# Performance work log

Hardware: AMD Instinct MI355X
Metric: run time of the kernel (lower is better)

Reference implementation:

```python
import jax, jax.numpy as jnp
import numpy as np

# Fixed topology: layer sizes input I, hidden H, output O; memory size M.
B, T, I, H, O, M = 64, 512, 256, 512, 256, 256
HALF = H // 2  # units 0..HALF-1 -> relu, HALF..H-1 -> tanh (activation ids 1 and 3)


def setup_inputs() -> dict:
    key = jax.random.key(0)
    ks = jax.random.split(key, 17)
    w = lambda k, shape: jax.random.normal(k, shape, dtype=jnp.float32) * 0.05
    return {
        "inputs": jax.random.normal(ks[0], (B, T, I), dtype=jnp.float32),
        # computation-graph edge weights (torch Linear: W @ x + b, W is (out,in))
        "W01": w(ks[1], (H, I)), "b01": w(ks[2], (H,)),
        "W12": w(ks[3], (O, H)), "b12": w(ks[4], (O,)),
        # memory -> layer projections
        "Wm0": w(ks[5], (I, M)), "bm0": w(ks[6], (I,)),
        "Wm1": w(ks[7], (H, M)), "bm1": w(ks[8], (H,)),
        "Wm2": w(ks[9], (O, M)), "bm2": w(ks[10], (O,)),
        # layer -> memory projections
        "W0m": w(ks[11], (M, I)), "b0m": w(ks[12], (M,)),
        "W1m": w(ks[13], (M, H)), "b1m": w(ks[14], (M,)),
        "W2m": w(ks[15], (M, O)), "b2m": w(ks[16], (M,)),
    }


def reference(inputs, W01, b01, W12, b12, Wm0, bm0, Wm1, bm1, Wm2, bm2,
              W0m, b0m, W1m, b1m, W2m, b2m):
    def step(mem, x_t):
        # layer 0 (input layer): add incoming memory, identity activation
        v0 = x_t + mem @ Wm0.T + bm0                      # (B, I)
        mem_out = v0 @ W0m.T + b0m                        # (B, M)
        # edge 0 -> 1, then layer 1: add memory, indexed activations
        v1 = v0 @ W01.T + b01 + mem @ Wm1.T + bm1         # (B, H)
        v1 = jnp.concatenate(
            [jax.nn.relu(v1[:, :HALF]), jnp.tanh(v1[:, HALF:])], axis=-1)
        mem_out = mem_out + v1 @ W1m.T + b1m
        # edge 1 -> 2, then layer 2 (output): add memory, identity activation
        v2 = v1 @ W12.T + b12 + mem @ Wm2.T + bm2         # (B, O)
        mem_out = mem_out + v2 @ W2m.T + b2m
        return mem_out, v2

    mem0 = jnp.zeros((inputs.shape[0], M), dtype=inputs.dtype)
    xs = jnp.swapaxes(inputs, 0, 1)                       # (T, B, I)
    mem_final, ys = jax.lax.scan(step, mem0, xs)
    outputs = jnp.swapaxes(ys, 0, 1)                      # (B, T, O)
    return outputs, mem_final
```

## Files before the change

kernel.cpp:

```cpp
#include <hip/hip_runtime.h>
#include <math.h>

#define BB 64
#define TT 512
#define II 256
#define HH 512
#define OO 256
#define MM 256
#define BT (BB*TT)

#define OFF_UA  0
#define OFF_W1S (BT*768)
#define OFF_W2R (OFF_W1S + HH*MM)
#define OFF_WYS (OFF_W2R + MM*768)
#define OFF_C1  (OFF_WYS + OO*768)
#define OFF_C2  (OFF_C1 + HH)
#define OFF_C3  (OFF_C2 + OO)
#define WS_FLOATS (OFF_C3 + MM)

__device__ __forceinline__ int w1s_index(int h, int k) {
    int p = h >> 1, r = h & 1;
    int ks = k >> 6, rem = k & 63;
    int j = rem >> 2, e = rem & 3;
    int tid = (p << 2) | ks;
    return OFF_W1S + ((j*2 + r)*1024 + tid)*4 + e;
}
__device__ __forceinline__ int w2r_index(int m, int k) {
    int ks = k / 192, jj = (k - 192*ks) >> 2, e = k & 3;
    int tid = (m << 2) | ks;
    return OFF_W2R + (jj*1024 + tid)*4 + e;
}

__global__ void pre_vecs(const float* __restrict__ W01, const float* __restrict__ b01,
                         const float* __restrict__ b12, const float* __restrict__ bm0,
                         const float* __restrict__ bm1, const float* __restrict__ bm2,
                         const float* __restrict__ W0m, const float* __restrict__ b0m,
                         const float* __restrict__ b1m, const float* __restrict__ b2m,
                         const float* __restrict__ W2m, float* __restrict__ ws) {
    int id = blockIdx.x*256 + threadIdx.x;
    if (id < HH) {
        float acc = b01[id] + bm1[id];
        for (int i = 0; i < II; ++i) acc += W01[id*II + i] * bm0[i];
        ws[OFF_C1 + id] = acc;
    } else if (id < HH + OO) {
        int m = id - HH;
        ws[OFF_C2 + m] = b12[m] + bm2[m];
        float acc = b0m[m] + b1m[m] + b2m[m];
        for (int i = 0; i < II; ++i) acc += W0m[m*II + i] * bm0[i];
        for (int o = 0; o < OO; ++o) acc += W2m[m*OO + o] * (b12[o] + bm2[o]);
        ws[OFF_C3 + m] = acc;
    }
}

__global__ void make_W1S(const float* __restrict__ W01, const float* __restrict__ Wm0,
                         const float* __restrict__ Wm1, float* __restrict__ ws) {
    int h = blockIdx.x, k = threadIdx.x;
    float acc = Wm1[h*MM + k];
    for (int i = 0; i < II; ++i) acc += W01[h*II + i] * Wm0[i*MM + k];
    ws[w1s_index(h, k)] = acc;
}
__global__ void make_A2(const float* __restrict__ W1m, const float* __restrict__ W2m,
                        const float* __restrict__ W12, float* __restrict__ ws) {
    int m = blockIdx.x, h = threadIdx.x;
    float acc = W1m[m*HH + h];
    for (int o = 0; o < OO; ++o) acc += W2m[m*OO + o] * W12[o*HH + h];
    ws[w2r_index(m, h)] = acc;
}
__global__ void make_A3(const float* __restrict__ W0m, const float* __restrict__ Wm0,
                        const float* __restrict__ W2m, const float* __restrict__ Wm2,
                        float* __restrict__ ws) {
    int m = blockIdx.x, m2 = threadIdx.x;
    float acc = 0.f;
    for (int i = 0; i < II; ++i) acc += W0m[m*II + i] * Wm0[i*MM + m2];
    for (int o = 0; o < OO; ++o) acc += W2m[m*OO + o] * Wm2[o*MM + m2];
    ws[w2r_index(m, 512 + m2)] = acc;
}
__global__ void make_WYS(const float* __restrict__ W12, const float* __restrict__ Wm2,
                         float* __restrict__ ws) {
    int o = blockIdx.x, k = threadIdx.x;
    ws[OFF_WYS + o*768 + k] = (k < HH) ? W12[o*HH + k] : Wm2[o*MM + (k - HH)];
}

template<int K4>
__global__ __launch_bounds__(256)
void gemm_nt(const float* __restrict__ x, int ldx4,
             const float* __restrict__ W, int ldw4,
             const float* __restrict__ cvec,
             float* __restrict__ out, int ldo4) {
    const int tid = threadIdx.x;
    const int tx = tid & 15, ty = tid >> 4;
    const int n0 = blockIdx.x * 64 + 4*ty;
    const int c0 = blockIdx.y * 64 + 4*tx;
    const float4* x4 = reinterpret_cast<const float4*>(x) + (size_t)n0*ldx4;
    const float4* W4 = reinterpret_cast<const float4*>(W) + (size_t)c0*ldw4;
    float acc[4][4] = {};
    #pragma unroll 4
    for (int k4 = 0; k4 < K4; ++k4) {
        float4 a[4], w[4];
        #pragma unroll
        for (int r = 0; r < 4; ++r) a[r] = x4[(size_t)r*ldx4 + k4];
        #pragma unroll
        for (int c = 0; c < 4; ++c) w[c] = W4[(size_t)c*ldw4 + k4];
        #pragma unroll
        for (int r = 0; r < 4; ++r)
            #pragma unroll
            for (int c = 0; c < 4; ++c)
                acc[r][c] += a[r].x*w[c].x + a[r].y*w[c].y + a[r].z*w[c].z + a[r].w*w[c].w;
    }
    #pragma unroll
    for (int r = 0; r < 4; ++r) {
        float4 o;
        o.x = acc[r][0] + cvec[c0+0];
        o.y = acc[r][1] + cvec[c0+1];
        o.z = acc[r][2] + cvec[c0+2];
        o.w = acc[r][3] + cvec[c0+3];
        reinterpret_cast<float4*>(out)[(size_t)(n0 + r)*ldo4 + (c0>>2)] = o;
    }
}

__device__ __forceinline__ float dot4(float4 w, float4 a) {
    return w.x*a.x + w.y*a.y + w.z*a.z + w.w*a.w;
}

__global__ __launch_bounds__(1024, 4)
void rnn_main(float* __restrict__ ws, float* __restrict__ out) {
    __shared__ float buf[2][816];
    __shared__ float4 lds_w[8*1024];
    const int tid = threadIdx.x;
    const int b = blockIdx.x;
    const int q = tid >> 2;
    const int ks = tid & 3;
    const bool lead = (ks == 0);

    const float4* W1S4 = reinterpret_cast<const float4*>(ws + OFF_W1S);
    const float4* W2R4 = reinterpret_cast<const float4*>(ws + OFF_W2R);
    float* UAb = ws + OFF_UA + (size_t)b*TT*768;

    float4 w1e[4], w1o[4];
    #pragma unroll
    for (int j = 0; j < 4; ++j) {
        w1e[j] = W1S4[(2*j)*1024 + tid];
        w1o[j] = W1S4[(2*j+1)*1024 + tid];
    }
    #pragma unroll
    for (int j = 0; j < 8; ++j) lds_w[j*1024 + tid] = W2R4[j*1024 + tid];
    if (tid < 256) { int k = 512 + tid; buf[0][k + ((k>>6)<<2)] = 0.f; }
    __syncthreads();

    for (int t = 0; t < TT; ++t) {
        const int p = t & 1;
        const float4* bufp4 = reinterpret_cast<const float4*>(buf[p]);
        float* row = UAb + (size_t)t*768;

        float2 u1 = make_float2(0.f, 0.f);
        float u0 = 0.f;
        if (lead) {
            u1 = *reinterpret_cast<const float2*>(row + 2*q);
            u0 = row[512 + q];
        }
        float a0 = 0.f, a1 = 0.f;
        #pragma unroll
        for (int j = 0; j < 4; ++j) {
            float4 a = bufp4[136 + 17*ks + j];
            a0 += dot4(w1e[j], a);
            a1 += dot4(w1o[j], a);
        }
        #pragma unroll 4
        for (int j = 4; j < 16; ++j) {
            float4 a  = bufp4[136 + 17*ks + j];
            float4 we = W1S4[(2*j)*1024 + tid];
            float4 wo = W1S4[(2*j+1)*1024 + tid];
            a0 += dot4(we, a);
            a1 += dot4(wo, a);
        }
        a0 += __shfl_xor(a0, 1); a0 += __shfl_xor(a0, 2);
        a1 += __shfl_xor(a1, 1); a1 += __shfl_xor(a1, 2);
        if (lead) {
            int h0 = 2*q;
            float v0 = a0 + u1.x, v1v = a1 + u1.y;
            if (h0 < 256) { v0 = fmaxf(v0, 0.f); v1v = fmaxf(v1v, 0.f); }
            else          { v0 = tanhf(v0);      v1v = tanhf(v1v); }
            int ai = h0 + ((h0>>6)<<2);
            *reinterpret_cast<float2*>(&buf[p][ai]) = make_float2(v0, v1v);
        }
        __syncthreads();

        float am = 0.f;
        #pragma unroll
        for (int jj = 0; jj < 8; ++jj) {
            float4 a = bufp4[51*ks + jj];
            am += dot4(lds_w[jj*1024 + tid], a);
        }
        if (tid < 384) {
            int k2 = 2*tid;
            float2 v = *reinterpret_cast<const float2*>(&buf[p][k2 + ((k2>>6)<<2)]);
            *reinterpret_cast<float2*>(row + k2) = v;
        }
        #pragma unroll 4
        for (int jj = 8; jj < 48; ++jj) {
            float4 a = bufp4[51*ks + jj + (jj>>4)];
            am += dot4(W2R4[jj*1024 + tid], a);
        }
        am += __shfl_xor(am, 1); am += __shfl_xor(am, 2);
        if (lead) {
            float mv = am + u0;
            int k = 512 + q;
            buf[p^1][k + ((k>>6)<<2)] = mv;
            if (t == TT-1) out[(size_t)BT*OO + b*MM + q] = mv;
        }
        __syncthreads();
    }
}

extern "C" void kernel_launch(void* const* d_in, const int* in_sizes, int n_in,
                              void* d_out, int out_size, void* d_ws, size_t ws_size,
                              hipStream_t stream) {
    const float* inputs = (const float*)d_in[0];
    const float* W01 = (const float*)d_in[1];  const float* b01 = (const float*)d_in[2];
    const float* W12 = (const float*)d_in[3];  const float* b12 = (const float*)d_in[4];
    const float* Wm0 = (const float*)d_in[5];  const float* bm0 = (const float*)d_in[6];
    const float* Wm1 = (const float*)d_in[7];  const float* bm1 = (const float*)d_in[8];
    const float* Wm2 = (const float*)d_in[9];  const float* bm2 = (const float*)d_in[10];
    const float* W0m = (const float*)d_in[11]; const float* b0m = (const float*)d_in[12];
    const float* W1m = (const float*)d_in[13]; const float* b1m = (const float*)d_in[14];
    const float* W2m = (const float*)d_in[15]; const float* b2m = (const float*)d_in[16];
    float* outf = (float*)d_out;
    float* wsf = (float*)d_ws;

    if (ws_size < (size_t)WS_FLOATS * sizeof(float)) return;

    pre_vecs<<<3, 256, 0, stream>>>(W01, b01, b12, bm0, bm1, bm2, W0m, b0m, b1m, b2m, W2m, wsf);
    make_W1S<<<HH, 256, 0, stream>>>(W01, Wm0, Wm1, wsf);
    make_A2<<<MM, 512, 0, stream>>>(W1m, W2m, W12, wsf);
    make_A3<<<MM, 256, 0, stream>>>(W0m, Wm0, W2m, Wm2, wsf);
    make_WYS<<<OO, 768, 0, stream>>>(W12, Wm2, wsf);
    gemm_nt<64><<<dim3(BT/64, HH/64), 256, 0, stream>>>(inputs, 64, W01, 64, wsf + OFF_C1, wsf + OFF_UA, 192);
    gemm_nt<64><<<dim3(BT/64, MM/64), 256, 0, stream>>>(inputs, 64, W0m, 64, wsf + OFF_C3, wsf + OFF_UA + 512, 192);
    rnn_main<<<BB, 1024, 0, stream>>>(wsf, outf);
    gemm_nt<192><<<dim3(BT/64, OO/64), 256, 0, stream>>>(wsf + OFF_UA, 192, wsf + OFF_WYS, 192, wsf + OFF_C2, outf, 64);
}
```

Before: 6.255 ms.

## Replace register-tiled GEMMs with LDS-tiled 128x128 GEMM and cache more recurrent weights

The three dense GEMMs (input projections and output projection) move from a 64x64 register-only tile that reads operands straight from global memory to a 128x128 tile staged through shared memory, with 8x8 outputs per thread. The goal is more operand reuse and less global traffic. Separately, the recurrent kernel keeps one more W2R slice in LDS (9 instead of 8) and preloads 8 more slices into registers, so fewer weight rows are re-read from global memory each timestep. The cost is higher register pressure in rnn_main at 1024 threads, which may cause spills, plus extra LDS use in both kernels.

```diff
diff --git a/kernel.cpp b/kernel.cpp
--- a/kernel.cpp
+++ b/kernel.cpp
@@ -81,40 +81,56 @@
     ws[OFF_WYS + o*768 + k] = (k < HH) ? W12[o*HH + k] : Wm2[o*MM + (k - HH)];
 }
 
-template<int K4>
+#define GS 22
+template<int K>
 __global__ __launch_bounds__(256)
-void gemm_nt(const float* __restrict__ x, int ldx4,
-             const float* __restrict__ W, int ldw4,
-             const float* __restrict__ cvec,
-             float* __restrict__ out, int ldo4) {
+void gemm_lds(const float* __restrict__ x, int ldx,
+              const float* __restrict__ W, int ldw,
+              const float* __restrict__ cvec,
+              float* __restrict__ out, int ldo) {
+    __shared__ float xs[128*GS];
+    __shared__ float wsh[128*GS];
     const int tid = threadIdx.x;
-    const int tx = tid & 15, ty = tid >> 4;
-    const int n0 = blockIdx.x * 64 + 4*ty;
-    const int c0 = blockIdx.y * 64 + 4*tx;
-    const float4* x4 = reinterpret_cast<const float4*>(x) + (size_t)n0*ldx4;
-    const float4* W4 = reinterpret_cast<const float4*>(W) + (size_t)c0*ldw4;
-    float acc[4][4] = {};
-    #pragma unroll 4
-    for (int k4 = 0; k4 < K4; ++k4) {
-        float4 a[4], w[4];
-        #pragma unroll
-        for (int r = 0; r < 4; ++r) a[r] = x4[(size_t)r*ldx4 + k4];
-        #pragma unroll
-        for (int c = 0; c < 4; ++c) w[c] = W4[(size_t)c*ldw4 + k4];
-        #pragma unroll
-        for (int r = 0; r < 4; ++r)
+    const int cx = tid & 15, cy = tid >> 4;
+    const int n0 = blockIdx.x * 128;
+    const int c0 = blockIdx.y * 128;
+    const int lrow = tid >> 2;
+    const int lk4 = tid & 3;
+    float acc[8][8] = {};
+    for (int k0 = 0; k0 < K; k0 += 16) {
+        #pragma unroll
+        for (int h = 0; h < 2; ++h) {
+            int r = lrow + 64*h;
+            float4 vx = *reinterpret_cast<const float4*>(&x[(size_t)(n0 + r)*ldx + k0 + 4*lk4]);
+            float4 vw = *reinterpret_cast<const float4*>(&W[(size_t)(c0 + r)*ldw + k0 + 4*lk4]);
+            int base = r*GS + 4*lk4;
+            xs[base+0]=vx.x; xs[base+1]=vx.y; xs[base+2]=vx.z; xs[base+3]=vx.w;
+            wsh[base+0]=vw.x; wsh[base+1]=vw.y; wsh[base+2]=vw.z; wsh[base+3]=vw.w;
+        }
+        __syncthreads();
+        #pragma unroll
+        for (int k = 0; k < 16; k += 2) {
+            float2 a[8], w[8];
             #pragma unroll
-            for (int c = 0; c < 4; ++c)
-                acc[r][c] += a[r].x*w[c].x + a[r].y*w[c].y + a[r].z*w[c].z + a[r].w*w[c].w;
-    }
-    #pragma unroll
-    for (int r = 0; r < 4; ++r) {
-        float4 o;
-        o.x = acc[r][0] + cvec[c0+0];
-        o.y = acc[r][1] + cvec[c0+1];
-        o.z = acc[r][2] + cvec[c0+2];
-        o.w = acc[r][3] + cvec[c0+3];
-        reinterpret_cast<float4*>(out)[(size_t)(n0 + r)*ldo4 + (c0>>2)] = o;
+            for (int j = 0; j < 8; ++j) a[j] = *reinterpret_cast<const float2*>(&xs[(cy + 16*j)*GS + k]);
+            #pragma unroll
+            for (int i = 0; i < 8; ++i) w[i] = *reinterpret_cast<const float2*>(&wsh[(cx + 16*i)*GS + k]);
+            #pragma unroll
+            for (int j = 0; j < 8; ++j)
+                #pragma unroll
+                for (int i = 0; i < 8; ++i)
+                    acc[j][i] += a[j].x*w[i].x + a[j].y*w[i].y;
+        }
+        __syncthreads();
+    }
+    #pragma unroll
+    for (int j = 0; j < 8; ++j) {
+        int n = n0 + cy + 16*j;
+        #pragma unroll
+        for (int i = 0; i < 8; ++i) {
+            int c = c0 + cx + 16*i;
+            out[(size_t)n*ldo + c] = acc[j][i] + cvec[c];
+        }
     }
 }
 
@@ -125,7 +141,7 @@
 __global__ __launch_bounds__(1024, 4)
 void rnn_main(float* __restrict__ ws, float* __restrict__ out) {
     __shared__ float buf[2][816];
-    __shared__ float4 lds_w[8*1024];
+    __shared__ float4 lds_w[9*1024];
     const int tid = threadIdx.x;
     const int b = blockIdx.x;
     const int q = tid >> 2;
@@ -142,8 +158,11 @@
         w1e[j] = W1S4[(2*j)*1024 + tid];
         w1o[j] = W1S4[(2*j+1)*1024 + tid];
     }
-    #pragma unroll
-    for (int j = 0; j < 8; ++j) lds_w[j*1024 + tid] = W2R4[j*1024 + tid];
+    float4 w2reg[8];
+    #pragma unroll
+    for (int i = 0; i < 8; ++i) w2reg[i] = W2R4[(9+i)*1024 + tid];
+    #pragma unroll
+    for (int j = 0; j < 9; ++j) lds_w[j*1024 + tid] = W2R4[j*1024 + tid];
     if (tid < 256) { int k = 512 + tid; buf[0][k + ((k>>6)<<2)] = 0.f; }
     __syncthreads();
 
@@ -187,9 +206,15 @@
 
         float am = 0.f;
         #pragma unroll
-        for (int jj = 0; jj < 8; ++jj) {
+        for (int jj = 0; jj < 9; ++jj) {
             float4 a = bufp4[51*ks + jj];
             am += dot4(lds_w[jj*1024 + tid], a);
+        }
+        #pragma unroll
+        for (int i = 0; i < 8; ++i) {
+            int jj = 9 + i;
+            float4 a = bufp4[51*ks + jj + (jj>>4)];
+            am += dot4(w2reg[i], a);
         }
         if (tid < 384) {
             int k2 = 2*tid;
@@ -197,7 +222,7 @@
             *reinterpret_cast<float2*>(row + k2) = v;
         }
         #pragma unroll 4
-        for (int jj = 8; jj < 48; ++jj) {
+        for (int jj = 17; jj < 48; ++jj) {
             float4 a = bufp4[51*ks + jj + (jj>>4)];
             am += dot4(W2R4[jj*1024 + tid], a);
         }
@@ -234,8 +259,8 @@
     make_A2<<<MM, 512, 0, stream>>>(W1m, W2m, W12, wsf);
     make_A3<<<MM, 256, 0, stream>>>(W0m, Wm0, W2m, Wm2, wsf);
     make_WYS<<<OO, 768, 0, stream>>>(W12, Wm2, wsf);
-    gemm_nt<64><<<dim3(BT/64, HH/64), 256, 0, stream>>>(inputs, 64, W01, 64, wsf + OFF_C1, wsf + OFF_UA, 192);
-    gemm_nt<64><<<dim3(BT/64, MM/64), 256, 0, stream>>>(inputs, 64, W0m, 64, wsf + OFF_C3, wsf + OFF_UA + 512, 192);
+    gemm_lds<II><<<dim3(BT/128, HH/128), 256, 0, stream>>>(inputs, II, W01, II, wsf + OFF_C1, wsf + OFF_UA, 768);
+    gemm_lds<II><<<dim3(BT/128, MM/128), 256, 0, stream>>>(inputs, II, W0m, II, wsf + OFF_C3, wsf + OFF_UA + 512, 768);
     rnn_main<<<BB, 1024, 0, stream>>>(wsf, outf);
-    gemm_nt<192><<<dim3(BT/64, OO/64), 256, 0, stream>>>(wsf + OFF_UA, 192, wsf + OFF_WYS, 192, wsf + OFF_C2, outf, 64);
-}
+    gemm_lds<768><<<dim3(BT/128, OO/128), 256, 0, stream>>>(wsf + OFF_UA, 768, wsf + OFF_WYS, 768, wsf + OFF_C2, outf, OO);
+}
```

After: 9.741 ms. +55.7%, slower.
